# Kernel optimization log

Measured on AMD Instinct MI355X. Metric: run time of the kernel, lower is better.

Reference implementation:

```python
import jax, jax.numpy as jnp
import numpy as np

B, S, D = 4, 2048, 768
LN_EPS = 1e-12


def setup_inputs() -> dict:
    key = jax.random.key(0)
    k0, k1, k2, k3 = jax.random.split(key, 4)
    scale = 1.0 / np.sqrt(D).astype(np.float32)
    return {
        "hidden_states": jax.random.normal(k0, (B, S, D), jnp.float32),
        "attention_mask": jnp.ones((B, 1, S, S), jnp.int32),
        "prior_n_attn": jax.random.uniform(k1, (B, S, S), jnp.float32),
        "ln_w": jnp.ones((D,), jnp.float32),
        "ln_b": jnp.zeros((D,), jnp.float32),
        "wq": jax.random.normal(k2, (D, D), jnp.float32) * scale,
        "bq": jnp.zeros((D,), jnp.float32),
        "wk": jax.random.normal(k3, (D, D), jnp.float32) * scale,
        "bk": jnp.zeros((D,), jnp.float32),
    }


def reference(hidden_states, attention_mask, prior_n_attn, ln_w, ln_b, wq, bq, wk, bk):
    _, S_, D_ = hidden_states.shape
    # LayerNorm (biased variance, as torch.nn.LayerNorm)
    mu = hidden_states.mean(-1, keepdims=True)
    var = ((hidden_states - mu) ** 2).mean(-1, keepdims=True)
    h = (hidden_states - mu) / jnp.sqrt(var + LN_EPS) * ln_w + ln_b

    a = jnp.eye(S_, k=1, dtype=jnp.int32)      # superdiagonal
    bI = jnp.eye(S_, dtype=jnp.int32)          # diagonal
    c = jnp.eye(S_, k=-1, dtype=jnp.int32)     # subdiagonal
    tri = jnp.triu(jnp.ones((S_, S_), jnp.float32))

    # mask & (a + c): band of width 1 off the diagonal; then squeeze dim 1
    mask = (attention_mask.astype(jnp.int32) & (a + c))[:, 0]  # [B,S,S]

    q = h @ wq + bq
    k = h @ wk + bk
    scores = jnp.einsum("bsd,btd->bst", q, k) / D_
    scores = jnp.where(mask == 0, -jnp.inf, scores)
    n = jnp.nan_to_num(jax.nn.softmax(scores, axis=-1))
    n = jnp.sqrt(n * jnp.swapaxes(n, -2, -1) + 1e-9)
    n = prior_n_attn + (1.0 - prior_n_attn) * n

    # keep only the superdiagonal of log(n + 1e-9); zero elsewhere
    logm = jnp.log(n + 1e-9) * a.astype(n.dtype)
    # prefix-sum via triangular matmuls (same math as torch source)
    t = logm @ tri                                   # [B,S,S]
    g = jnp.exp(jnp.einsum("ij,bjk->bik", tri, t))   # [B,S,S]
    su = tri - bI.astype(tri.dtype)                  # strictly-upper indicator
    g = g * su                                       # masked_fill((tri-b)==0, 0)
    diag_part = jnp.where(bI == 0, 1e-9, n)          # n.masked_fill(b==0, 1e-9)
    g = g + jnp.swapaxes(g, -2, -1) + diag_part
    return (g, n)
```

## Files before the change

### kernel.cpp

```cpp
#include <hip/hip_runtime.h>
#include <hip/hip_bf16.h>
#include <math.h>
#include <stdint.h>

#define BB 4
#define SS 2048
#define DD 768
#define MM (BB*SS)

typedef __attribute__((ext_vector_type(4))) float  f32x4;
typedef __attribute__((ext_vector_type(8))) __bf16 bf16x8;
typedef __attribute__((ext_vector_type(4))) __bf16 bf16x4;

#define AS1 __attribute__((address_space(1)))
#define AS3 __attribute__((address_space(3)))

__global__ __launch_bounds__(256) void prep_kernel(const float* __restrict__ wq,
        const float* __restrict__ wk, const float* __restrict__ bq,
        const float* __restrict__ bk, __bf16* __restrict__ G,
        float* __restrict__ u, float* __restrict__ v, float* __restrict__ cb) {
    __shared__ __attribute__((aligned(16))) __bf16 As[128][32];
    __shared__ __attribute__((aligned(16))) __bf16 Bs[128][32];
    const int bid = blockIdx.x;
    if (bid >= 36) {
        const int id = bid - 36;
        const int lane = threadIdx.x & 63, wv_ = threadIdx.x >> 6;
        if (id == 384) {
            if (wv_ != 0) return;
            float s = 0.f;
#pragma unroll
            for (int m = 0; m < 12; m++) s += bq[lane + 64 * m] * bk[lane + 64 * m];
#pragma unroll
            for (int o = 1; o < 64; o <<= 1) s += __shfl_xor(s, o);
            if (lane == 0) cb[0] = s;
            return;
        }
        const bool isU = id < 192;
        const int row = (isU ? id : id - 192) * 4 + wv_;
        const float* W = isU ? wq : wk;
        const float* bvec = isU ? bk : bq;
        const float* wr_ = W + (size_t)row * DD;
        float s = 0.f;
#pragma unroll
        for (int m = 0; m < 12; m++) s += wr_[lane + 64 * m] * bvec[lane + 64 * m];
#pragma unroll
        for (int o = 1; o < 64; o <<= 1) s += __shfl_xor(s, o);
        if (lane == 0) (isU ? u : v)[row] = s;
        return;
    }
    const int m0 = (bid % 6) * 128;
    const int n0 = (bid / 6) * 128;
    const int t = threadIdx.x;
    const int wave = t >> 6, lane = t & 63;
    const int wr = wave >> 1, wc = wave & 1;
    const int srow = t >> 1, shalf = (t & 1) * 16;
    f32x4 acc[4][4] = {};

    for (int k0 = 0; k0 < DD; k0 += 32) {
        const float* ga = wq + (size_t)(m0 + srow) * DD + k0 + shalf;
        const float* gb = wk + (size_t)(n0 + srow) * DD + k0 + shalf;
        f32x4 a0 = *(const f32x4*)(ga),     a1 = *(const f32x4*)(ga + 4);
        f32x4 a2 = *(const f32x4*)(ga + 8), a3 = *(const f32x4*)(ga + 12);
        f32x4 b0 = *(const f32x4*)(gb),     b1 = *(const f32x4*)(gb + 4);
        f32x4 b2 = *(const f32x4*)(gb + 8), b3 = *(const f32x4*)(gb + 12);
        bf16x8 av0, av1, bv0, bv1;
#pragma unroll
        for (int c = 0; c < 4; c++) {
            av0[c] = (__bf16)a0[c]; av0[4 + c] = (__bf16)a1[c];
            av1[c] = (__bf16)a2[c]; av1[4 + c] = (__bf16)a3[c];
            bv0[c] = (__bf16)b0[c]; bv0[4 + c] = (__bf16)b1[c];
            bv1[c] = (__bf16)b2[c]; bv1[4 + c] = (__bf16)b3[c];
        }
        __syncthreads();
        *(bf16x8*)&As[srow][shalf]     = av0;
        *(bf16x8*)&As[srow][shalf + 8] = av1;
        *(bf16x8*)&Bs[srow][shalf]     = bv0;
        *(bf16x8*)&Bs[srow][shalf + 8] = bv1;
        __syncthreads();
        const int r = lane & 15, ko = (lane >> 4) << 3;
        bf16x8 af[4], bvf[4];
#pragma unroll
        for (int i = 0; i < 4; i++) af[i]  = *(const bf16x8*)&As[wr * 64 + i * 16 + r][ko];
#pragma unroll
        for (int j = 0; j < 4; j++) bvf[j] = *(const bf16x8*)&Bs[wc * 64 + j * 16 + r][ko];
#pragma unroll
        for (int i = 0; i < 4; i++)
#pragma unroll
            for (int j = 0; j < 4; j++)
                acc[i][j] = __builtin_amdgcn_mfma_f32_16x16x32_bf16(af[i], bvf[j], acc[i][j], 0, 0, 0);
    }
#pragma unroll
    for (int i = 0; i < 4; i++) {
        const int mm = m0 + wr * 64 + i * 16 + (lane >> 4) * 4;
#pragma unroll
        for (int j = 0; j < 4; j++) {
            const int nn = n0 + wc * 64 + j * 16 + (lane & 15);
#pragma unroll
            for (int rr = 0; rr < 4; rr++)
                G[(size_t)(mm + rr) * DD + nn] = (__bf16)acc[i][j][rr];
        }
    }
}

__global__ __launch_bounds__(256) void ln_kernel(const float* __restrict__ x,
        const float* __restrict__ lw, const float* __restrict__ lb,
        const float* __restrict__ v, const float* __restrict__ cbp,
        __bf16* __restrict__ h, float* __restrict__ Barr) {
    const int row = blockIdx.x * 4 + (threadIdx.x >> 6);
    const int lane = threadIdx.x & 63;
    const float* xr = x + (size_t)row * DD + lane * 12;
    f32x4 a0 = *(const f32x4*)(xr), a1 = *(const f32x4*)(xr + 4), a2 = *(const f32x4*)(xr + 8);
    float xs[12];
#pragma unroll
    for (int c = 0; c < 4; c++) { xs[c] = a0[c]; xs[4 + c] = a1[c]; xs[8 + c] = a2[c]; }
    float s = 0.f, ss = 0.f;
#pragma unroll
    for (int c = 0; c < 12; c++) { s += xs[c]; ss += xs[c] * xs[c]; }
#pragma unroll
    for (int o = 1; o < 64; o <<= 1) { s += __shfl_xor(s, o); ss += __shfl_xor(ss, o); }
    const float mu = s * (1.0f / DD);
    const float var = ss * (1.0f / DD) - mu * mu;
    const float rstd = 1.0f / sqrtf(var + 1e-12f);
    const float* wp = lw + lane * 12; const float* bp = lb + lane * 12;
    const float* vp = v + lane * 12;
    f32x4 w0 = *(const f32x4*)(wp), w1 = *(const f32x4*)(wp + 4), w2 = *(const f32x4*)(wp + 8);
    f32x4 b0 = *(const f32x4*)(bp), b1 = *(const f32x4*)(bp + 4), b2 = *(const f32x4*)(bp + 8);
    f32x4 v0 = *(const f32x4*)(vp), v1 = *(const f32x4*)(vp + 4), v2 = *(const f32x4*)(vp + 8);
    float wv[12], bv[12], vv[12];
#pragma unroll
    for (int c = 0; c < 4; c++) {
        wv[c] = w0[c]; wv[4 + c] = w1[c]; wv[8 + c] = w2[c];
        bv[c] = b0[c]; bv[4 + c] = b1[c]; bv[8 + c] = b2[c];
        vv[c] = v0[c]; vv[4 + c] = v1[c]; vv[8 + c] = v2[c];
    }
    bf16x4 o0, o1, o2;
    float bpv = 0.f;
#pragma unroll
    for (int c = 0; c < 12; c++) {
        const float y = (xs[c] - mu) * rstd * wv[c] + bv[c];
        bpv += y * vv[c];
        if (c < 4) o0[c] = (__bf16)y; else if (c < 8) o1[c - 4] = (__bf16)y; else o2[c - 8] = (__bf16)y;
    }
    __bf16* hr = h + (size_t)row * DD + lane * 12;
    *(bf16x4*)(hr) = o0; *(bf16x4*)(hr + 4) = o1; *(bf16x4*)(hr + 8) = o2;
#pragma unroll
    for (int o = 1; o < 64; o <<= 1) bpv += __shfl_xor(bpv, o);
    if (lane == 0) Barr[row] = bpv + cbp[0];
}

__global__ __launch_bounds__(256) void rgemm_kernel(const __bf16* __restrict__ A,
        const __bf16* __restrict__ Bt, const float* __restrict__ u,
        __bf16* __restrict__ C) {
    __shared__ __attribute__((aligned(16))) __bf16 As[128][32];
    __shared__ __attribute__((aligned(16))) __bf16 Bs[128][32];
    const int m0 = blockIdx.x * 128;
    const int n0 = blockIdx.y * 128;
    const int t = threadIdx.x;
    const int wave = t >> 6, lane = t & 63;
    const int wr = wave >> 1, wc = wave & 1;
    f32x4 acc[4][4] = {};

    char* asb = (char*)&As[0][0];
    char* bsb = (char*)&Bs[0][0];
    const int c0  = wave * 64 + lane;
    const int rA0 = c0 >> 2;
    const int cA0 = (c0 & 3) << 3;

    for (int k0 = 0; k0 < DD; k0 += 32) {
        const __bf16* ga0 = A  + (size_t)(m0 + rA0) * DD + k0 + cA0;
        const __bf16* ga1 = ga0 + (size_t)64 * DD;
        const __bf16* gb0 = Bt + (size_t)(n0 + rA0) * DD + k0 + cA0;
        const __bf16* gb1 = gb0 + (size_t)64 * DD;
        __builtin_amdgcn_global_load_lds((const AS1 void*)(ga0), (AS3 void*)(asb + wave * 1024),        16, 0, 0);
        __builtin_amdgcn_global_load_lds((const AS1 void*)(ga1), (AS3 void*)(asb + 4096 + wave * 1024), 16, 0, 0);
        __builtin_amdgcn_global_load_lds((const AS1 void*)(gb0), (AS3 void*)(bsb + wave * 1024),        16, 0, 0);
        __builtin_amdgcn_global_load_lds((const AS1 void*)(gb1), (AS3 void*)(bsb + 4096 + wave * 1024), 16, 0, 0);
        __syncthreads();
        const int r = lane & 15, ko = (lane >> 4) << 3;
        bf16x8 af[4], bvf[4];
#pragma unroll
        for (int i = 0; i < 4; i++) af[i]  = *(const bf16x8*)&As[wr * 64 + i * 16 + r][ko];
#pragma unroll
        for (int j = 0; j < 4; j++) bvf[j] = *(const bf16x8*)&Bs[wc * 64 + j * 16 + r][ko];
#pragma unroll
        for (int i = 0; i < 4; i++)
#pragma unroll
            for (int j = 0; j < 4; j++)
                acc[i][j] = __builtin_amdgcn_mfma_f32_16x16x32_bf16(af[i], bvf[j], acc[i][j], 0, 0, 0);
        __syncthreads();
    }
#pragma unroll
    for (int i = 0; i < 4; i++) {
        const int mm = m0 + wr * 64 + i * 16 + (lane >> 4) * 4;
#pragma unroll
        for (int j = 0; j < 4; j++) {
            const int nn = n0 + wc * 64 + j * 16 + (lane & 15);
            const float bias = u[nn];
#pragma unroll
            for (int rr = 0; rr < 4; rr++)
                C[(size_t)(mm + rr) * DD + nn] = (__bf16)(acc[i][j][rr] + bias);
        }
    }
}

__global__ __launch_bounds__(256) void band_kernel(const __bf16* __restrict__ h,
        const __bf16* __restrict__ R, const int* __restrict__ att,
        const float* __restrict__ Barr, const float* __restrict__ prior,
        float* __restrict__ pu, float* __restrict__ pd, float* __restrict__ prsup) {
    const int idx  = blockIdx.x * 4 + (threadIdx.x >> 6);
    const int lane = threadIdx.x & 63;
    const int b = idx >> 11;
    const int s = idx & 2047;
    if (lane == 1 && s < SS - 1)
        prsup[idx] = prior[((size_t)b * SS + s) * SS + s + 1];
    const __bf16* hp = h + (size_t)idx * DD + lane * 12;
    bf16x4 h0 = *(const bf16x4*)(hp), h1 = *(const bf16x4*)(hp + 4), h2 = *(const bf16x4*)(hp + 8);
    float hv[12];
#pragma unroll
    for (int c = 0; c < 4; c++) { hv[c] = (float)h0[c]; hv[4 + c] = (float)h1[c]; hv[8 + c] = (float)h2[c]; }
    float du = 0.f, dn = 0.f;
    if (s < SS - 1) {
        const __bf16* rp = R + (size_t)(idx + 1) * DD + lane * 12;
        bf16x4 r0 = *(const bf16x4*)(rp), r1 = *(const bf16x4*)(rp + 4), r2 = *(const bf16x4*)(rp + 8);
#pragma unroll
        for (int c = 0; c < 4; c++) {
            du += hv[c] * (float)r0[c];
            du += hv[4 + c] * (float)r1[c];
            du += hv[8 + c] * (float)r2[c];
        }
    }
    if (s > 0) {
        const __bf16* rp = R + (size_t)(idx - 1) * DD + lane * 12;
        bf16x4 r0 = *(const bf16x4*)(rp), r1 = *(const bf16x4*)(rp + 4), r2 = *(const bf16x4*)(rp + 8);
#pragma unroll
        for (int c = 0; c < 4; c++) {
            dn += hv[c] * (float)r0[c];
            dn += hv[4 + c] * (float)r1[c];
            dn += hv[8 + c] * (float)r2[c];
        }
    }
#pragma unroll
    for (int o = 1; o < 64; o <<= 1) { du += __shfl_xor(du, o); dn += __shfl_xor(dn, o); }
    if (lane == 0) {
        const float eu = (du + ((s < SS - 1) ? Barr[idx + 1] : 0.f)) * (1.0f / DD);
        const float ed = (dn + ((s > 0)      ? Barr[idx - 1] : 0.f)) * (1.0f / DD);
        const bool au = (s < SS - 1) && ((att[((size_t)b * SS + s) * SS + (s + 1)] & 1) != 0);
        const bool ad = (s > 0)      && ((att[((size_t)b * SS + s) * SS + (s - 1)] & 1) != 0);
        float puv = 0.f, pdv = 0.f;
        if (au || ad) {
            float mx = au ? eu : ed;
            if (au && ad) mx = fmaxf(eu, ed);
            const float zu = au ? expf(eu - mx) : 0.f;
            const float zd = ad ? expf(ed - mx) : 0.f;
            const float iz = 1.f / (zu + zd);
            puv = zu * iz; pdv = zd * iz;
        }
        pu[idx] = puv; pd[idx] = pdv;
    }
}

__global__ __launch_bounds__(256) void scan_kernel(const float* __restrict__ pu,
        const float* __restrict__ pd, const float* __restrict__ prsup,
        float* __restrict__ nb, double* __restrict__ P2) {
    const int b = blockIdx.x;
    const int t = threadIdx.x;
    double L[8];
    double mysum = 0.0;
#pragma unroll
    for (int e = 0; e < 8; e++) {
        const int s = t * 8 + e;
        double Lv = 0.0;
        float nbv = 0.f;
        if (s < SS - 1) {
            const float a = pu[b * SS + s];
            const float c = pd[b * SS + s + 1];
            nbv = sqrtf(a * c + 1e-9f);
            const float pr = prsup[b * SS + s];
            const float nsup = pr + (1.f - pr) * nbv;
            Lv = (double)log2f(nsup + 1e-9f);
        }
        nb[b * SS + s] = nbv;
        L[e] = Lv; mysum += Lv;
    }
    __shared__ double warr[256];
    warr[t] = mysum;
    __syncthreads();
    for (int o = 1; o < 256; o <<= 1) {
        double v = 0.0;
        if (t >= o) v = warr[t - o];
        __syncthreads();
        if (t >= o) warr[t] += v;
        __syncthreads();
    }
    double run = warr[t] - mysum;
#pragma unroll
    for (int e = 0; e < 8; e++) {
        P2[(size_t)b * SS + t * 8 + e] = run;
        run += L[e];
    }
}

__global__ __launch_bounds__(256) void out_kernel(const float* __restrict__ prior,
        const float* __restrict__ nb, const double* __restrict__ P2,
        float* __restrict__ gout, float* __restrict__ nout) {
    const size_t t8 = (size_t)blockIdx.x * 256 + threadIdx.x;
    const int b = (int)(t8 >> 19);
    const size_t off = t8 << 3;
    const size_t r = off & ((1u << 22) - 1);
    const int i  = (int)(r >> 11);
    const int k0 = (int)(r & 2047);
    const f32x4 p0 = *(const f32x4*)(prior + off);
    const f32x4 p1 = *(const f32x4*)(prior + off + 4);
    const double* Pb = P2 + ((size_t)b << 11);
    const double Pi = Pb[i];
    const float* nbb = nb + ((size_t)b << 11);
    f32x4 g0, g1, n0, n1;
#pragma unroll
    for (int c = 0; c < 8; c++) {
        const int k = k0 + c;
        const float pr = (c < 4) ? p0[c] : p1[c - 4];
        float vv = 3.16227766016838e-5f;
        if (k == i + 1)      vv = nbb[i];
        else if (k == i - 1) vv = nbb[k];
        const float nval = pr + (1.f - pr) * vv;
        float g;
        if (k == i) {
            g = nval;
        } else {
            const double Pk = Pb[k];
            const double dd = (k > i) ? (Pk - Pi) : (Pi - Pk);
            g = exp2f((float)dd) + 1e-9f;
        }
        if (c < 4) { g0[c] = g; n0[c] = nval; }
        else       { g1[c - 4] = g; n1[c - 4] = nval; }
    }
    *(f32x4*)(gout + off)     = g0;
    *(f32x4*)(gout + off + 4) = g1;
    *(f32x4*)(nout + off)     = n0;
    *(f32x4*)(nout + off + 4) = n1;
}

extern "C" void kernel_launch(void* const* d_in, const int* in_sizes, int n_in,
                              void* d_out, int out_size, void* d_ws, size_t ws_size,
                              hipStream_t stream) {
    const float* hs    = (const float*)d_in[0];
    const int*   att   = (const int*)d_in[1];
    const float* prior = (const float*)d_in[2];
    const float* ln_w  = (const float*)d_in[3];
    const float* ln_b  = (const float*)d_in[4];
    const float* wq    = (const float*)d_in[5];
    const float* bq    = (const float*)d_in[6];
    const float* wk    = (const float*)d_in[7];
    const float* bk    = (const float*)d_in[8];

    float* gout = (float*)d_out;
    float* nout = gout + (size_t)BB * SS * SS;

    char* ws = (char*)d_ws;
    __bf16* h     = (__bf16*)(ws);
    __bf16* G     = (__bf16*)(ws + 12582912);
    __bf16* R     = (__bf16*)(ws + 13762560);
    float*  u     = (float*) (ws + 26345472);
    float*  v     = (float*) (ws + 26348544);
    float*  cbp   = (float*) (ws + 26351616);
    float*  Barr  = (float*) (ws + 26351872);
    float*  pu    = (float*) (ws + 26384640);
    float*  pd    = (float*) (ws + 26417408);
    float*  nbuf  = (float*) (ws + 26450176);
    float*  prsup = (float*) (ws + 26482944);
    double* P2    = (double*)(ws + 26515712);

    prep_kernel<<<dim3(421), dim3(256), 0, stream>>>(wq, wk, bq, bk, G, u, v, cbp);
    ln_kernel<<<dim3(MM / 4), dim3(256), 0, stream>>>(hs, ln_w, ln_b, v, cbp, h, Barr);
    rgemm_kernel<<<dim3(MM / 128, 6), dim3(256), 0, stream>>>(h, G, u, R);
    band_kernel<<<dim3(MM / 4), dim3(256), 0, stream>>>(h, R, att, Barr, prior, pu, pd, prsup);
    scan_kernel<<<dim3(BB), dim3(256), 0, stream>>>(pu, pd, prsup, nbuf, P2);
    out_kernel<<<dim3((BB * SS * SS / 8) / 256), dim3(256), 0, stream>>>(prior, nbuf, P2, gout, nout);
}
```

Baseline: 120.4 us.

## Merge LayerNorm into weight-prep launch and move softmax into scan

The LayerNorm kernel is folded into the weight-prep kernel as extra blocks, so one launch runs both and two weight-dependent reductions no longer serialize with LN. The bias dot term (h·v) moves from the LN stage into the band kernel. The band-softmax moves into the single-block scan kernel, which keeps pd in shared memory instead of writing and rereading pu and pd. The prep GEMM tile shrinks to 64x64 to give more blocks, and the rgemm grid is transposed so that consecutive blocks share the same A rows. The trade-off is that the serial scan kernel does more work per block and band writes four arrays.

```diff
diff --git a/kernel.cpp b/kernel.cpp
--- a/kernel.cpp
+++ b/kernel.cpp
@@ -15,15 +15,48 @@
 #define AS1 __attribute__((address_space(1)))
 #define AS3 __attribute__((address_space(3)))
 
-__global__ __launch_bounds__(256) void prep_kernel(const float* __restrict__ wq,
+__global__ __launch_bounds__(256) void combined_kernel(
+        const float* __restrict__ x, const float* __restrict__ lw,
+        const float* __restrict__ lb, const float* __restrict__ wq,
         const float* __restrict__ wk, const float* __restrict__ bq,
         const float* __restrict__ bk, __bf16* __restrict__ G,
-        float* __restrict__ u, float* __restrict__ v, float* __restrict__ cb) {
-    __shared__ __attribute__((aligned(16))) __bf16 As[128][32];
-    __shared__ __attribute__((aligned(16))) __bf16 Bs[128][32];
+        float* __restrict__ u, float* __restrict__ v, float* __restrict__ cb,
+        __bf16* __restrict__ h) {
+    __shared__ __attribute__((aligned(16))) __bf16 As[64][32];
+    __shared__ __attribute__((aligned(16))) __bf16 Bs[64][32];
     const int bid = blockIdx.x;
-    if (bid >= 36) {
-        const int id = bid - 36;
+    if (bid >= 529) {
+        const int row = (bid - 529) * 4 + (threadIdx.x >> 6);
+        const int lane = threadIdx.x & 63;
+        const float* xr = x + (size_t)row * DD + lane * 12;
+        f32x4 a0 = *(const f32x4*)(xr), a1 = *(const f32x4*)(xr + 4), a2 = *(const f32x4*)(xr + 8);
+        float xs[12];
+#pragma unroll
+        for (int c = 0; c < 4; c++) { xs[c] = a0[c]; xs[4 + c] = a1[c]; xs[8 + c] = a2[c]; }
+        float s = 0.f, ss = 0.f;
+#pragma unroll
+        for (int c = 0; c < 12; c++) { s += xs[c]; ss += xs[c] * xs[c]; }
+#pragma unroll
+        for (int o = 1; o < 64; o <<= 1) { s += __shfl_xor(s, o); ss += __shfl_xor(ss, o); }
+        const float mu = s * (1.0f / DD);
+        const float var = ss * (1.0f / DD) - mu * mu;
+        const float rstd = 1.0f / sqrtf(var + 1e-12f);
+        const float* wp = lw + lane * 12; const float* bp = lb + lane * 12;
+        f32x4 w0 = *(const f32x4*)(wp), w1 = *(const f32x4*)(wp + 4), w2 = *(const f32x4*)(wp + 8);
+        f32x4 b0 = *(const f32x4*)(bp), b1 = *(const f32x4*)(bp + 4), b2 = *(const f32x4*)(bp + 8);
+        bf16x4 o0, o1, o2;
+#pragma unroll
+        for (int c = 0; c < 4; c++) {
+            o0[c] = (__bf16)((xs[c]     - mu) * rstd * w0[c] + b0[c]);
+            o1[c] = (__bf16)((xs[4 + c] - mu) * rstd * w1[c] + b1[c]);
+            o2[c] = (__bf16)((xs[8 + c] - mu) * rstd * w2[c] + b2[c]);
+        }
+        __bf16* hr = h + (size_t)row * DD + lane * 12;
+        *(bf16x4*)(hr) = o0; *(bf16x4*)(hr + 4) = o1; *(bf16x4*)(hr + 8) = o2;
+        return;
+    }
+    if (bid >= 144) {
+        const int id = bid - 144;
         const int lane = threadIdx.x & 63, wv_ = threadIdx.x >> 6;
         if (id == 384) {
             if (wv_ != 0) return;
@@ -48,104 +81,52 @@
         if (lane == 0) (isU ? u : v)[row] = s;
         return;
     }
-    const int m0 = (bid % 6) * 128;
-    const int n0 = (bid / 6) * 128;
+    const int m0 = (bid % 12) * 64;
+    const int n0 = (bid / 12) * 64;
     const int t = threadIdx.x;
     const int wave = t >> 6, lane = t & 63;
     const int wr = wave >> 1, wc = wave & 1;
-    const int srow = t >> 1, shalf = (t & 1) * 16;
-    f32x4 acc[4][4] = {};
+    const int srow = t >> 2, scol = (t & 3) * 8;
+    f32x4 acc[2][2] = {};
 
     for (int k0 = 0; k0 < DD; k0 += 32) {
-        const float* ga = wq + (size_t)(m0 + srow) * DD + k0 + shalf;
-        const float* gb = wk + (size_t)(n0 + srow) * DD + k0 + shalf;
-        f32x4 a0 = *(const f32x4*)(ga),     a1 = *(const f32x4*)(ga + 4);
-        f32x4 a2 = *(const f32x4*)(ga + 8), a3 = *(const f32x4*)(ga + 12);
-        f32x4 b0 = *(const f32x4*)(gb),     b1 = *(const f32x4*)(gb + 4);
-        f32x4 b2 = *(const f32x4*)(gb + 8), b3 = *(const f32x4*)(gb + 12);
-        bf16x8 av0, av1, bv0, bv1;
+        const float* ga = wq + (size_t)(m0 + srow) * DD + k0 + scol;
+        const float* gb = wk + (size_t)(n0 + srow) * DD + k0 + scol;
+        f32x4 a0 = *(const f32x4*)(ga), a1 = *(const f32x4*)(ga + 4);
+        f32x4 b0 = *(const f32x4*)(gb), b1 = *(const f32x4*)(gb + 4);
+        bf16x8 av, bv;
 #pragma unroll
         for (int c = 0; c < 4; c++) {
-            av0[c] = (__bf16)a0[c]; av0[4 + c] = (__bf16)a1[c];
-            av1[c] = (__bf16)a2[c]; av1[4 + c] = (__bf16)a3[c];
-            bv0[c] = (__bf16)b0[c]; bv0[4 + c] = (__bf16)b1[c];
-            bv1[c] = (__bf16)b2[c]; bv1[4 + c] = (__bf16)b3[c];
-        }
-        __syncthreads();
-        *(bf16x8*)&As[srow][shalf]     = av0;
-        *(bf16x8*)&As[srow][shalf + 8] = av1;
-        *(bf16x8*)&Bs[srow][shalf]     = bv0;
-        *(bf16x8*)&Bs[srow][shalf + 8] = bv1;
+            av[c] = (__bf16)a0[c]; av[4 + c] = (__bf16)a1[c];
+            bv[c] = (__bf16)b0[c]; bv[4 + c] = (__bf16)b1[c];
+        }
+        __syncthreads();
+        *(bf16x8*)&As[srow][scol] = av;
+        *(bf16x8*)&Bs[srow][scol] = bv;
         __syncthreads();
         const int r = lane & 15, ko = (lane >> 4) << 3;
-        bf16x8 af[4], bvf[4];
-#pragma unroll
-        for (int i = 0; i < 4; i++) af[i]  = *(const bf16x8*)&As[wr * 64 + i * 16 + r][ko];
-#pragma unroll
-        for (int j = 0; j < 4; j++) bvf[j] = *(const bf16x8*)&Bs[wc * 64 + j * 16 + r][ko];
-#pragma unroll
-        for (int i = 0; i < 4; i++)
-#pragma unroll
-            for (int j = 0; j < 4; j++)
+        bf16x8 af[2], bvf[2];
+#pragma unroll
+        for (int i = 0; i < 2; i++) af[i]  = *(const bf16x8*)&As[wr * 32 + i * 16 + r][ko];
+#pragma unroll
+        for (int j = 0; j < 2; j++) bvf[j] = *(const bf16x8*)&Bs[wc * 32 + j * 16 + r][ko];
+#pragma unroll
+        for (int i = 0; i < 2; i++)
+#pragma unroll
+            for (int j = 0; j < 2; j++)
                 acc[i][j] = __builtin_amdgcn_mfma_f32_16x16x32_bf16(af[i], bvf[j], acc[i][j], 0, 0, 0);
     }
 #pragma unroll
-    for (int i = 0; i < 4; i++) {
-        const int mm = m0 + wr * 64 + i * 16 + (lane >> 4) * 4;
-#pragma unroll
-        for (int j = 0; j < 4; j++) {
-            const int nn = n0 + wc * 64 + j * 16 + (lane & 15);
+    for (int i = 0; i < 2; i++) {
+        const int mm = m0 + wr * 32 + i * 16 + (lane >> 4) * 4;
+#pragma unroll
+        for (int j = 0; j < 2; j++) {
+            const int nn = n0 + wc * 32 + j * 16 + (lane & 15);
 #pragma unroll
             for (int rr = 0; rr < 4; rr++)
                 G[(size_t)(mm + rr) * DD + nn] = (__bf16)acc[i][j][rr];
         }
     }
-}
-
-__global__ __launch_bounds__(256) void ln_kernel(const float* __restrict__ x,
-        const float* __restrict__ lw, const float* __restrict__ lb,
-        const float* __restrict__ v, const float* __restrict__ cbp,
-        __bf16* __restrict__ h, float* __restrict__ Barr) {
-    const int row = blockIdx.x * 4 + (threadIdx.x >> 6);
-    const int lane = threadIdx.x & 63;
-    const float* xr = x + (size_t)row * DD + lane * 12;
-    f32x4 a0 = *(const f32x4*)(xr), a1 = *(const f32x4*)(xr + 4), a2 = *(const f32x4*)(xr + 8);
-    float xs[12];
-#pragma unroll
-    for (int c = 0; c < 4; c++) { xs[c] = a0[c]; xs[4 + c] = a1[c]; xs[8 + c] = a2[c]; }
-    float s = 0.f, ss = 0.f;
-#pragma unroll
-    for (int c = 0; c < 12; c++) { s += xs[c]; ss += xs[c] * xs[c]; }
-#pragma unroll
-    for (int o = 1; o < 64; o <<= 1) { s += __shfl_xor(s, o); ss += __shfl_xor(ss, o); }
-    const float mu = s * (1.0f / DD);
-    const float var = ss * (1.0f / DD) - mu * mu;
-    const float rstd = 1.0f / sqrtf(var + 1e-12f);
-    const float* wp = lw + lane * 12; const float* bp = lb + lane * 12;
-    const float* vp = v + lane * 12;
-    f32x4 w0 = *(const f32x4*)(wp), w1 = *(const f32x4*)(wp + 4), w2 = *(const f32x4*)(wp + 8);
-    f32x4 b0 = *(const f32x4*)(bp), b1 = *(const f32x4*)(bp + 4), b2 = *(const f32x4*)(bp + 8);
-    f32x4 v0 = *(const f32x4*)(vp), v1 = *(const f32x4*)(vp + 4), v2 = *(const f32x4*)(vp + 8);
-    float wv[12], bv[12], vv[12];
-#pragma unroll
-    for (int c = 0; c < 4; c++) {
-        wv[c] = w0[c]; wv[4 + c] = w1[c]; wv[8 + c] = w2[c];
-        bv[c] = b0[c]; bv[4 + c] = b1[c]; bv[8 + c] = b2[c];
-        vv[c] = v0[c]; vv[4 + c] = v1[c]; vv[8 + c] = v2[c];
-    }
-    bf16x4 o0, o1, o2;
-    float bpv = 0.f;
-#pragma unroll
-    for (int c = 0; c < 12; c++) {
-        const float y = (xs[c] - mu) * rstd * wv[c] + bv[c];
-        bpv += y * vv[c];
-        if (c < 4) o0[c] = (__bf16)y; else if (c < 8) o1[c - 4] = (__bf16)y; else o2[c - 8] = (__bf16)y;
-    }
-    __bf16* hr = h + (size_t)row * DD + lane * 12;
-    *(bf16x4*)(hr) = o0; *(bf16x4*)(hr + 4) = o1; *(bf16x4*)(hr + 8) = o2;
-#pragma unroll
-    for (int o = 1; o < 64; o <<= 1) bpv += __shfl_xor(bpv, o);
-    if (lane == 0) Barr[row] = bpv + cbp[0];
 }
 
 __global__ __launch_bounds__(256) void rgemm_kernel(const __bf16* __restrict__ A,
@@ -153,8 +134,8 @@
         __bf16* __restrict__ C) {
     __shared__ __attribute__((aligned(16))) __bf16 As[128][32];
     __shared__ __attribute__((aligned(16))) __bf16 Bs[128][32];
-    const int m0 = blockIdx.x * 128;
-    const int n0 = blockIdx.y * 128;
+    const int m0 = blockIdx.y * 128;
+    const int n0 = blockIdx.x * 128;
     const int t = threadIdx.x;
     const int wave = t >> 6, lane = t & 63;
     const int wr = wave >> 1, wc = wave & 1;
@@ -205,8 +186,10 @@
 
 __global__ __launch_bounds__(256) void band_kernel(const __bf16* __restrict__ h,
         const __bf16* __restrict__ R, const int* __restrict__ att,
-        const float* __restrict__ Barr, const float* __restrict__ prior,
-        float* __restrict__ pu, float* __restrict__ pd, float* __restrict__ prsup) {
+        const float* __restrict__ v, const float* __restrict__ cbp,
+        const float* __restrict__ prior,
+        float* __restrict__ du_o, float* __restrict__ dn_o, float* __restrict__ w_o,
+        int* __restrict__ fl_o, float* __restrict__ prsup) {
     const int idx  = blockIdx.x * 4 + (threadIdx.x >> 6);
     const int lane = threadIdx.x & 63;
     const int b = idx >> 11;
@@ -218,36 +201,60 @@
     float hv[12];
 #pragma unroll
     for (int c = 0; c < 4; c++) { hv[c] = (float)h0[c]; hv[4 + c] = (float)h1[c]; hv[8 + c] = (float)h2[c]; }
-    float du = 0.f, dn = 0.f;
+    const float* vp = v + lane * 12;
+    f32x4 v0 = *(const f32x4*)(vp), v1 = *(const f32x4*)(vp + 4), v2 = *(const f32x4*)(vp + 8);
+    float du = 0.f, dn = 0.f, w = 0.f;
+#pragma unroll
+    for (int c = 0; c < 4; c++) {
+        w += hv[c] * v0[c] + hv[4 + c] * v1[c] + hv[8 + c] * v2[c];
+    }
     if (s < SS - 1) {
         const __bf16* rp = R + (size_t)(idx + 1) * DD + lane * 12;
         bf16x4 r0 = *(const bf16x4*)(rp), r1 = *(const bf16x4*)(rp + 4), r2 = *(const bf16x4*)(rp + 8);
 #pragma unroll
-        for (int c = 0; c < 4; c++) {
-            du += hv[c] * (float)r0[c];
-            du += hv[4 + c] * (float)r1[c];
-            du += hv[8 + c] * (float)r2[c];
-        }
+        for (int c = 0; c < 4; c++)
+            du += hv[c] * (float)r0[c] + hv[4 + c] * (float)r1[c] + hv[8 + c] * (float)r2[c];
     }
     if (s > 0) {
         const __bf16* rp = R + (size_t)(idx - 1) * DD + lane * 12;
         bf16x4 r0 = *(const bf16x4*)(rp), r1 = *(const bf16x4*)(rp + 4), r2 = *(const bf16x4*)(rp + 8);
 #pragma unroll
-        for (int c = 0; c < 4; c++) {
-            dn += hv[c] * (float)r0[c];
-            dn += hv[4 + c] * (float)r1[c];
-            dn += hv[8 + c] * (float)r2[c];
-        }
-    }
-#pragma unroll
-    for (int o = 1; o < 64; o <<= 1) { du += __shfl_xor(du, o); dn += __shfl_xor(dn, o); }
+        for (int c = 0; c < 4; c++)
+            dn += hv[c] * (float)r0[c] + hv[4 + c] * (float)r1[c] + hv[8 + c] * (float)r2[c];
+    }
+#pragma unroll
+    for (int o = 1; o < 64; o <<= 1) {
+        du += __shfl_xor(du, o); dn += __shfl_xor(dn, o); w += __shfl_xor(w, o);
+    }
     if (lane == 0) {
-        const float eu = (du + ((s < SS - 1) ? Barr[idx + 1] : 0.f)) * (1.0f / DD);
-        const float ed = (dn + ((s > 0)      ? Barr[idx - 1] : 0.f)) * (1.0f / DD);
         const bool au = (s < SS - 1) && ((att[((size_t)b * SS + s) * SS + (s + 1)] & 1) != 0);
         const bool ad = (s > 0)      && ((att[((size_t)b * SS + s) * SS + (s - 1)] & 1) != 0);
+        du_o[idx] = du;
+        dn_o[idx] = dn;
+        w_o[idx]  = w + cbp[0];
+        fl_o[idx] = (au ? 1 : 0) | (ad ? 2 : 0);
+    }
+}
+
+__global__ __launch_bounds__(256) void scan_kernel(const float* __restrict__ du_i,
+        const float* __restrict__ dn_i, const float* __restrict__ w_i,
+        const int* __restrict__ fl_i, const float* __restrict__ prsup,
+        float* __restrict__ nb, double* __restrict__ P2) {
+    const int b = blockIdx.x;
+    const int t = threadIdx.x;
+    __shared__ float sh_pd[SS];
+    __shared__ double warr[256];
+    float pu_r[8];
+#pragma unroll
+    for (int e = 0; e < 8; e++) {
+        const int s = t * 8 + e;
+        const int idx = b * SS + s;
+        const int fl = fl_i[idx];
+        const bool au = fl & 1, ad = fl & 2;
         float puv = 0.f, pdv = 0.f;
         if (au || ad) {
+            const float eu = au ? (du_i[idx] + w_i[idx + 1]) * (1.0f / DD) : 0.f;
+            const float ed = ad ? (dn_i[idx] + w_i[idx - 1]) * (1.0f / DD) : 0.f;
             float mx = au ? eu : ed;
             if (au && ad) mx = fmaxf(eu, ed);
             const float zu = au ? expf(eu - mx) : 0.f;
@@ -255,15 +262,10 @@
             const float iz = 1.f / (zu + zd);
             puv = zu * iz; pdv = zd * iz;
         }
-        pu[idx] = puv; pd[idx] = pdv;
-    }
-}
-
-__global__ __launch_bounds__(256) void scan_kernel(const float* __restrict__ pu,
-        const float* __restrict__ pd, const float* __restrict__ prsup,
-        float* __restrict__ nb, double* __restrict__ P2) {
-    const int b = blockIdx.x;
-    const int t = threadIdx.x;
+        pu_r[e] = puv;
+        sh_pd[s] = pdv;
+    }
+    __syncthreads();
     double L[8];
     double mysum = 0.0;
 #pragma unroll
@@ -272,9 +274,7 @@
         double Lv = 0.0;
         float nbv = 0.f;
         if (s < SS - 1) {
-            const float a = pu[b * SS + s];
-            const float c = pd[b * SS + s + 1];
-            nbv = sqrtf(a * c + 1e-9f);
+            nbv = sqrtf(pu_r[e] * sh_pd[s + 1] + 1e-9f);
             const float pr = prsup[b * SS + s];
             const float nsup = pr + (1.f - pr) * nbv;
             Lv = (double)log2f(nsup + 1e-9f);
@@ -282,14 +282,13 @@
         nb[b * SS + s] = nbv;
         L[e] = Lv; mysum += Lv;
     }
-    __shared__ double warr[256];
     warr[t] = mysum;
     __syncthreads();
     for (int o = 1; o < 256; o <<= 1) {
-        double v = 0.0;
-        if (t >= o) v = warr[t - o];
-        __syncthreads();
-        if (t >= o) warr[t] += v;
+        double vv = 0.0;
+        if (t >= o) vv = warr[t - o];
+        __syncthreads();
+        if (t >= o) warr[t] += vv;
         __syncthreads();
     }
     double run = warr[t] - mysum;
@@ -363,17 +362,17 @@
     float*  u     = (float*) (ws + 26345472);
     float*  v     = (float*) (ws + 26348544);
     float*  cbp   = (float*) (ws + 26351616);
-    float*  Barr  = (float*) (ws + 26351872);
-    float*  pu    = (float*) (ws + 26384640);
-    float*  pd    = (float*) (ws + 26417408);
-    float*  nbuf  = (float*) (ws + 26450176);
+    float*  du    = (float*) (ws + 26351872);
+    float*  dn    = (float*) (ws + 26384640);
+    float*  wv    = (float*) (ws + 26417408);
+    int*    fl    = (int*)   (ws + 26450176);
     float*  prsup = (float*) (ws + 26482944);
-    double* P2    = (double*)(ws + 26515712);
-
-    prep_kernel<<<dim3(421), dim3(256), 0, stream>>>(wq, wk, bq, bk, G, u, v, cbp);
-    ln_kernel<<<dim3(MM / 4), dim3(256), 0, stream>>>(hs, ln_w, ln_b, v, cbp, h, Barr);
-    rgemm_kernel<<<dim3(MM / 128, 6), dim3(256), 0, stream>>>(h, G, u, R);
-    band_kernel<<<dim3(MM / 4), dim3(256), 0, stream>>>(h, R, att, Barr, prior, pu, pd, prsup);
-    scan_kernel<<<dim3(BB), dim3(256), 0, stream>>>(pu, pd, prsup, nbuf, P2);
+    float*  nbuf  = (float*) (ws + 26515712);
+    double* P2    = (double*)(ws + 26548480);
+
+    combined_kernel<<<dim3(2577), dim3(256), 0, stream>>>(hs, ln_w, ln_b, wq, wk, bq, bk, G, u, v, cbp, h);
+    rgemm_kernel<<<dim3(6, MM / 128), dim3(256), 0, stream>>>(h, G, u, R);
+    band_kernel<<<dim3(MM / 4), dim3(256), 0, stream>>>(h, R, att, v, cbp, prior, du, dn, wv, fl, prsup);
+    scan_kernel<<<dim3(BB), dim3(256), 0, stream>>>(du, dn, wv, fl, prsup, nbuf, P2);
     out_kernel<<<dim3((BB * SS * SS / 8) / 256), dim3(256), 0, stream>>>(prior, nbuf, P2, gout, nout);
 }
```

Result: faster. 106.5 us (-11.6%).
